# Optimization experiments

Measured on AMD Instinct MI355X. Metric: run time of the kernel, lower is better.

The kernel has to match this reference:

```python
import jax, jax.numpy as jnp
import numpy as np

V, D, F, H, NB, S, B = 16384, 512, 2048, 8, 4, 512, 2
T_STEPS = 3      # config.T: number of PC inference iterations
GAMMA = 0.1      # state-update step size


def _layernorm(x, s, b):
    m = x.mean(-1, keepdims=True)
    v = ((x - m) ** 2).mean(-1, keepdims=True)
    return (x - m) * jax.lax.rsqrt(v + 1e-5) * s + b


def setup_inputs() -> dict:
    key = jax.random.key(0)
    ks = jax.random.split(key, 12)
    r = lambda k, sh: jax.random.normal(k, sh, jnp.float32) * 0.02
    return {
        'word_emb': r(ks[0], (V, D)),
        'pos_emb': r(ks[1], (S, D)),
        'Wq': r(ks[2], (NB, D, D)),
        'Wk': r(ks[3], (NB, D, D)),
        'Wv': r(ks[4], (NB, D, D)),
        'bq': jnp.zeros((NB, D), jnp.float32),
        'bk': jnp.zeros((NB, D), jnp.float32),
        'bv': jnp.zeros((NB, D), jnp.float32),
        'Wo': r(ks[5], (NB, D, D)),
        'bo': jnp.zeros((NB, D), jnp.float32),
        'ln1_s': jnp.ones((NB, D), jnp.float32),
        'ln1_b': jnp.zeros((NB, D), jnp.float32),
        'ln2_s': jnp.ones((NB, D), jnp.float32),
        'ln2_b': jnp.zeros((NB, D), jnp.float32),
        'W1': r(ks[6], (NB, D, F)),
        'b1': jnp.zeros((NB, F), jnp.float32),
        'W2': r(ks[7], (NB, F, D)),
        'b2': jnp.zeros((NB, D), jnp.float32),
        'Wout': r(ks[8], (D, V)),
        'bout': jnp.zeros((V,), jnp.float32),
        'input_ids': jax.random.randint(ks[9], (B, S), 0, V),
        'target_ids': jax.random.randint(ks[10], (B, S), 0, V),
    }


def _forward(word_emb, pos_emb, Wq, Wk, Wv, bq, bk, bv, Wo, bo,
             ln1_s, ln1_b, ln2_s, ln2_b, W1, b1, W2, b2, Wout, bout,
             input_ids, target_ids):
    Bsz, Sl = input_ids.shape
    dh = D // H
    scale = 1.0 / float(np.sqrt(dh))
    ids = jnp.clip(input_ids, 0, V - 1)
    target = jax.nn.one_hot(jnp.clip(target_ids, 0, V - 1), V, dtype=word_emb.dtype)
    # bottom prediction: word + position embeddings
    mu_emb = word_emb[ids] + pos_emb[jnp.arange(Sl)][None]  # (B,S,D)
    causal = jnp.tril(jnp.ones((Sl, Sl), bool))
    neg = jnp.finfo(word_emb.dtype).min

    def attn(x, b):
        h = _layernorm(x, ln1_s[b], ln1_b[b])
        q = (h @ Wq[b] + bq[b]).reshape(Bsz, Sl, H, dh)
        k = (h @ Wk[b] + bk[b]).reshape(Bsz, Sl, H, dh)
        v = (h @ Wv[b] + bv[b]).reshape(Bsz, Sl, H, dh)
        sc = jnp.einsum('bqhd,bkhd->bhqk', q, k) * scale
        sc = jnp.where(causal, sc, neg)
        a = jax.nn.softmax(sc, axis=-1)
        return jnp.einsum('bhqk,bkhd->bqhd', a, v).reshape(Bsz, Sl, D)

    # generative functions g[l]: x_l -> mu_{l+1}; 4 PC layers per block
    # (pc_qkv->attn ctx, pc_output->Wo, pc_layer1->gelu(fc1), pc_layer2->fc2)
    gs = []
    for b in range(NB):
        gs.append(lambda x, b=b: attn(x, b))
        gs.append(lambda x, b=b: x @ Wo[b] + bo[b])
        gs.append(lambda x, b=b: jax.nn.gelu(_layernorm(x, ln2_s[b], ln2_b[b]) @ W1[b] + b1[b]))
        gs.append(lambda x, b=b: x @ W2[b] + b2[b])
    g_top = lambda x: x @ Wout + bout  # output pc layer -> logits mu

    # init_x: forward sweep sets each latent to its prediction
    xs = [mu_emb]
    for g in gs:
        xs.append(g(xs[-1]))
    L = len(gs)

    # T-step iterative PC inference: eps_l = x_l - mu_l, top clamped to target
    # x_l <- x_l + GAMMA * (J_{g_l}(x_l)^T eps_{l+1} - eps_l)
    for _ in range(T_STEPS):
        preds, vjps = [], []
        for l in range(L):
            mu, vj = jax.vjp(gs[l], xs[l])
            preds.append(mu)
            vjps.append(vj)
        logits, vj_top = jax.vjp(g_top, xs[L])
        eps = [xs[0] - mu_emb] + [xs[l + 1] - preds[l] for l in range(L)]
        eps_top = logits - target
        new_xs = []
        for l in range(L + 1):
            td = vjps[l](eps[l + 1])[0] if l < L else vj_top(eps_top)[0]
            new_xs.append(xs[l] + GAMMA * (td - eps[l]))
        xs = new_xs

    return g_top(xs[L])  # get_mu('linear_output')


def reference(word_emb, pos_emb, Wq, Wk, Wv, bq, bk, bv, Wo, bo,
              ln1_s, ln1_b, ln2_s, ln2_b, W1, b1, W2, b2, Wout, bout,
              input_ids, target_ids):
    return _forward(word_emb, pos_emb, Wq, Wk, Wv, bq, bk, bv, Wo, bo,
                    ln1_s, ln1_b, ln2_s, ln2_b, W1, b1, W2, b2, Wout, bout,
                    input_ids, target_ids)
```

## Files before the change

### kernel.cpp

```cpp
#include <hip/hip_runtime.h>
#include <hip/hip_bf16.h>
#include <math.h>

#define D_   512
#define F_   2048
#define V_   16384
#define H_   8
#define DH_  64
#define S_   512
#define B_   2
#define M_   1024
#define MD_  (M_ * D_)
#define MF_  (M_ * F_)
#define GAMMA_ 0.1f

typedef unsigned int u32;
typedef unsigned short u16;
typedef __attribute__((ext_vector_type(4))) float f32x4;
typedef __attribute__((ext_vector_type(8))) short s16x8;
typedef __attribute__((ext_vector_type(4))) u16 u16x4;
typedef __attribute__((ext_vector_type(8))) u16 u16x8;

__device__ __forceinline__ u16 f2b(float f) {
    __hip_bfloat16 h = __float2bfloat16(f);
    return *reinterpret_cast<u16*>(&h);
}
__device__ __forceinline__ float b2f(u16 v) {
    u32 u = ((u32)v) << 16;
    float f; __builtin_memcpy(&f, &u, 4); return f;
}
__device__ __forceinline__ u16x4 pack4(f32x4 v) {
    u16x4 o; o.x = f2b(v[0]); o.y = f2b(v[1]); o.z = f2b(v[2]); o.w = f2b(v[3]);
    return o;
}

__device__ __forceinline__ void gl_lds16(const void* g, void* l) {
    __builtin_amdgcn_global_load_lds((const __attribute__((address_space(1))) u32*)g,
                                     (__attribute__((address_space(3))) u32*)l, 16, 0, 0);
}

__device__ __forceinline__ float gelu_f(float v) {
    float u = 0.7978845608028654f * (v + 0.044715f * v * v * v);
    return 0.5f * v * (1.f + tanhf(u));
}

__device__ __forceinline__ f32x4 xpose4(f32x4 v, int b) {
#pragma unroll
    for (int s = 1; s < 4; s <<= 1) {
        f32x4 nv;
#pragma unroll
        for (int j = 0; j < 4; ++j) {
            float ex = __shfl_xor(v[j ^ s], s, 64);
            nv[j] = ((b ^ j) & s) ? ex : v[j];
        }
        v = nv;
    }
    return v;
}

__device__ __forceinline__ float wave_sum(float v) {
#pragma unroll
    for (int o = 32; o > 0; o >>= 1) v += __shfl_xor(v, o, 64);
    return v;
}

#define E_F32   0
#define E_GELU  1
#define E_TD    2
#define E_EC2   3
#define E_QKV3  4
#define E_OUT   5
#define E_BF16  6

template<int BK>
__device__ __forceinline__ int swz(int c, int row) {
    if constexpr (BK == 32) return c ^ ((row >> 1) & 3);
    else                    return c ^ (row & 7);
}

template<int BM, int BN, int BK, int FM, int FN, int EPI>
__global__ __launch_bounds__(256)
void mfma_gemm(const u16* __restrict__ A, const u16* __restrict__ B,
               float* __restrict__ Cf, u16* __restrict__ Cb,
               u16* __restrict__ Cb2, u16* __restrict__ Cb3,
               const float* __restrict__ bias,
               int K, int lda, int ldb, int ldc,
               long sC, long sKz, float alpha,
               const float* __restrict__ base, const float* __restrict__ subv,
               const float* __restrict__ cvec, const u16* __restrict__ woutTb,
               const int* __restrict__ tcl,
               float* __restrict__ ebF, u16* __restrict__ ebB)
{
    constexpr int WC = BN / (FN * 16);
    static_assert((BM / (FM * 16)) * WC == 4, "4 waves");
    constexpr int LPR = BK / 8;
    constexpr int RPI = 2048 / BK;
    constexpr int NISS = BM / RPI + BN / RPI;
    __shared__ __align__(16) u16 Asl[3][BM * BK];
    __shared__ __align__(16) u16 Bsl[3][BN * BK];
    const int t = threadIdx.x, l = t & 63, wid = t >> 6;
    const int m0 = blockIdx.y * BM, n0 = blockIdx.x * BN;
    const long z = blockIdx.z;
    A += z * sKz;
    B += z * sKz;
    if (Cf) Cf += z * sC;

    f32x4 acc[FM][FN] = {};
    const int rm = (wid / WC) * (FM * 16), cn = (wid % WC) * (FN * 16);
    const int lr = l & 15, hi = l >> 4;
    const int srl = t / LPR, sc = t % LPR;

    auto stage = [&](int k0, int pb) {
#pragma unroll
        for (int i = 0; i < BM / RPI; ++i) {
            int row = i * RPI + srl;
            gl_lds16(A + (size_t)(m0 + row) * lda + k0 + swz<BK>(sc, row) * 8,
                     &Asl[pb][i * 2048 + t * 8]);
        }
#pragma unroll
        for (int i = 0; i < BN / RPI; ++i) {
            int row = i * RPI + srl;
            gl_lds16(B + (size_t)(n0 + row) * ldb + k0 + swz<BK>(sc, row) * 8,
                     &Bsl[pb][i * 2048 + t * 8]);
        }
    };
    auto compute = [&](int pb) {
#pragma unroll
        for (int kk = 0; kk < BK / 32; ++kk) {
            s16x8 av[FM], bv[FN];
#pragma unroll
            for (int fm = 0; fm < FM; ++fm)
                av[fm] = *(const s16x8*)&Asl[pb][(rm + fm * 16 + lr) * BK + swz<BK>(kk * 4 + hi, lr) * 8];
#pragma unroll
            for (int fn = 0; fn < FN; ++fn)
                bv[fn] = *(const s16x8*)&Bsl[pb][(cn + fn * 16 + lr) * BK + swz<BK>(kk * 4 + hi, lr) * 8];
#pragma unroll
            for (int fm = 0; fm < FM; ++fm)
#pragma unroll
                for (int fn = 0; fn < FN; ++fn)
                    acc[fm][fn] = __builtin_amdgcn_mfma_f32_16x16x32_bf16(av[fm], bv[fn], acc[fm][fn], 0, 0, 0);
        }
    };

    const int nst = K / BK;
    stage(0, 0);
    if (nst > 1) stage(BK, 1);
    int rd = 0, wr = 2;
    for (int s = 0; s < nst; ++s) {
        if (s < nst - 1)
            asm volatile("s_waitcnt vmcnt(%0)" :: "i"(NISS) : "memory");
        else
            asm volatile("s_waitcnt vmcnt(0)" ::: "memory");
        __builtin_amdgcn_s_barrier();
        __builtin_amdgcn_sched_barrier(0);
        compute(rd);
        if (s + 2 < nst) stage((s + 2) * BK, wr);
        rd = (rd + 1 == 3) ? 0 : rd + 1;
        wr = (wr + 1 == 3) ? 0 : wr + 1;
    }

    const int qb = lr & 3, qi = lr >> 2;
#pragma unroll
    for (int fm = 0; fm < FM; ++fm)
#pragma unroll
        for (int fn = 0; fn < FN; ++fn) {
            const int gm = m0 + rm + fm * 16 + hi * 4 + qb;
            const int gn0 = n0 + cn + fn * 16 + qi * 4;
            const size_t idx0 = (size_t)gm * ldc + gn0;
            if constexpr (EPI == E_QKV3) {
                const int gnf = n0 + cn + fn * 16;
                const int sel = gnf >> 9;
                if (sel < 2) {
                    f32x4 v = xpose4(acc[fm][fn], qb);
                    f32x4 bv4 = *(const f32x4*)&bias[gn0];
#pragma unroll
                    for (int j = 0; j < 4; ++j) v[j] += bv4[j];
                    int b = gm >> 9, s = gm & (S_ - 1);
                    int d9 = gn0 & 511, h = d9 >> 6, d = d9 & 63;
                    u16* dst = (sel == 0) ? Cb : Cb2;
                    *(u16x4*)&dst[(((size_t)(b * H_ + h) * S_ + s) << 6) + d] = pack4(v);
                } else {
                    const int gnl = gnf + lr;
                    const int gm0 = m0 + rm + fm * 16 + hi * 4;
                    int b = gm0 >> 9, s0 = gm0 & (S_ - 1);
                    int d9 = gnl & 511, h = d9 >> 6, d = d9 & 63;
                    float bb = bias[gnl];
                    f32x4 v = acc[fm][fn];
#pragma unroll
                    for (int j = 0; j < 4; ++j) v[j] += bb;
                    *(u16x4*)&Cb3[((((size_t)(b * H_ + h)) << 6) + d) * S_ + s0] = pack4(v);
                }
            } else {
                f32x4 v = xpose4(acc[fm][fn], qb);
                if constexpr (EPI == E_F32) {
#pragma unroll
                    for (int j = 0; j < 4; ++j) v[j] *= alpha;
                    if (bias) {
                        f32x4 bv4 = *(const f32x4*)&bias[gn0];
#pragma unroll
                        for (int j = 0; j < 4; ++j) v[j] += bv4[j];
                    }
                    *(f32x4*)&Cf[idx0] = v;
                    if (Cb) *(u16x4*)&Cb[idx0] = pack4(v);
                } else if constexpr (EPI == E_OUT) {
                    f32x4 bv4 = *(const f32x4*)&bias[gn0];
#pragma unroll
                    for (int j = 0; j < 4; ++j) v[j] += bv4[j];
                    *(f32x4*)&Cf[idx0] = v;
                } else if constexpr (EPI == E_GELU) {
                    f32x4 bv4 = *(const f32x4*)&bias[gn0];
#pragma unroll
                    for (int j = 0; j < 4; ++j) v[j] = gelu_f(v[j] + bv4[j]);
                    *(u16x4*)&Cb[idx0] = pack4(v);
                } else if constexpr (EPI == E_TD) {
                    const int tc = tcl[gm];
                    f32x4 cv4 = *(const f32x4*)&cvec[gn0];
                    f32x4 ba4 = *(const f32x4*)&base[idx0];
                    u16x4 gv = *(const u16x4*)&woutTb[(size_t)tc * D_ + gn0];
                    f32x4 dlt, o2;
#pragma unroll
                    for (int j = 0; j < 4; ++j)
                        dlt[j] = GAMMA_ * (v[j] + cv4[j] - b2f(gv[j]));
                    if (subv) {
                        f32x4 sv4 = *(const f32x4*)&subv[idx0];
#pragma unroll
                        for (int j = 0; j < 4; ++j) dlt[j] -= GAMMA_ * sv4[j];
                    }
#pragma unroll
                    for (int j = 0; j < 4; ++j) o2[j] = ba4[j] + dlt[j];
                    if (Cf) *(f32x4*)&Cf[idx0] = o2;
                    *(u16x4*)&Cb[idx0] = pack4(o2);
                    if (ebF) *(f32x4*)&ebF[idx0] = dlt;
                    if (ebB) *(u16x4*)&ebB[idx0] = pack4(dlt);
                } else if constexpr (EPI == E_EC2) {
                    f32x4 ba4 = *(const f32x4*)&base[idx0];
                    f32x4 sv4 = *(const f32x4*)&subv[idx0];
#pragma unroll
                    for (int j = 0; j < 4; ++j) v[j] = ba4[j] - sv4[j] - GAMMA_ * v[j];
                    *(f32x4*)&Cf[idx0] = v;
                } else if constexpr (EPI == E_BF16) {
                    *(u16x4*)&Cb[idx0] = pack4(v);
                }
            }
        }
}

__global__ __launch_bounds__(256)
void flash_attn(const u16* __restrict__ q, const u16* __restrict__ k,
                const u16* __restrict__ vT, u16* __restrict__ ctx)
{
    __shared__ __align__(16) u16 Ks[3][64 * 64];
    __shared__ __align__(16) u16 Vs[3][64 * 64];
    __shared__ __align__(16) u16 Ps[4][16 * 64];
    const int t = threadIdx.x, l = t & 63, w = t >> 6;
    const int qt = blockIdx.x, z = blockIdx.y;
    const int bb = z >> 3, hh = z & 7;
    const int lr = l & 15, hi = l >> 4;
    const u16* qp = q + (((size_t)z * S_ + qt * 64 + w * 16) << 6);
    const u16* kp = k + ((size_t)z * S_ << 6);
    const u16* vp = vT + (((size_t)z) << 6) * S_;

    const s16x8 aq0 = *(const s16x8*)&qp[lr * 64 + hi * 8];
    const s16x8 aq1 = *(const s16x8*)&qp[lr * 64 + 32 + hi * 8];

    f32x4 o[4] = {};
    float m[4], ls[4];
#pragma unroll
    for (int r = 0; r < 4; ++r) { m[r] = -3.0e38f; ls[r] = 0.f; }
    const int qrow = qt * 64 + w * 16 + hi * 4;
    const int srow = t >> 3, scl = t & 7;
    const int cg1 = (scl ^ (srow & 7)) * 8;
    const int srow2 = srow + 32;
    const int cg2 = (scl ^ (srow2 & 7)) * 8;
    const int sw7 = (lr & 7);

    auto stage = [&](int j, int pb) {
        gl_lds16(kp + ((size_t)(j * 64 + srow) << 6) + cg1, &Ks[pb][t * 8]);
        gl_lds16(vp + (size_t)srow * S_ + j * 64 + cg1, &Vs[pb][t * 8]);
        gl_lds16(kp + ((size_t)(j * 64 + srow2) << 6) + cg2, &Ks[pb][(t + 256) * 8]);
        gl_lds16(vp + (size_t)srow2 * S_ + j * 64 + cg2, &Vs[pb][(t + 256) * 8]);
    };

    stage(0, 0);
    if (qt > 0) stage(1, 1);
    int rd = 0, wr = 2;
    for (int j = 0; j <= qt; ++j) {
        if (j < qt) asm volatile("s_waitcnt vmcnt(4)" ::: "memory");
        else        asm volatile("s_waitcnt vmcnt(0)" ::: "memory");
        __builtin_amdgcn_s_barrier();
        __builtin_amdgcn_sched_barrier(0);

        float pv[4][4];
#pragma unroll
        for (int fn = 0; fn < 4; ++fn) {
            f32x4 acc = {};
            acc = __builtin_amdgcn_mfma_f32_16x16x32_bf16(aq0,
                    *(const s16x8*)&Ks[rd][((fn * 16 + lr) << 6) + ((hi ^ sw7) * 8)], acc, 0, 0, 0);
            acc = __builtin_amdgcn_mfma_f32_16x16x32_bf16(aq1,
                    *(const s16x8*)&Ks[rd][((fn * 16 + lr) << 6) + (((hi + 4) ^ sw7) * 8)], acc, 0, 0, 0);
#pragma unroll
            for (int r = 0; r < 4; ++r) pv[fn][r] = acc[r] * 0.125f;
        }
        if (j == qt) {
#pragma unroll
            for (int fn = 0; fn < 4; ++fn) {
                int col = j * 64 + fn * 16 + lr;
#pragma unroll
                for (int r = 0; r < 4; ++r)
                    if (col > qrow + r) pv[fn][r] = -3.0e38f;
            }
        }
        float sc[4], rs[4];
#pragma unroll
        for (int r = 0; r < 4; ++r) {
            float x = fmaxf(fmaxf(pv[0][r], pv[1][r]), fmaxf(pv[2][r], pv[3][r]));
#pragma unroll
            for (int off = 1; off < 16; off <<= 1) x = fmaxf(x, __shfl_xor(x, off, 64));
            float nm = fmaxf(m[r], x);
            sc[r] = expf(m[r] - nm);
            m[r] = nm;
            rs[r] = 0.f;
        }
#pragma unroll
        for (int fn = 0; fn < 4; ++fn)
#pragma unroll
            for (int r = 0; r < 4; ++r) {
                float p = expf(pv[fn][r] - m[r]);
                pv[fn][r] = p;
                rs[r] += p;
            }
#pragma unroll
        for (int r = 0; r < 4; ++r) {
#pragma unroll
            for (int off = 1; off < 16; off <<= 1) rs[r] += __shfl_xor(rs[r], off, 64);
            ls[r] = ls[r] * sc[r] + rs[r];
        }
#pragma unroll
        for (int fn = 0; fn < 4; ++fn)
#pragma unroll
            for (int r = 0; r < 4; ++r) o[fn][r] *= sc[r];
#pragma unroll
        for (int fn = 0; fn < 4; ++fn)
#pragma unroll
            for (int r = 0; r < 4; ++r) {
                int qr = hi * 4 + r;
                int ci = (2 * fn + (lr >> 3)) ^ (qr & 7);
                Ps[w][qr * 64 + ci * 8 + (lr & 7)] = f2b(pv[fn][r]);
            }
#pragma unroll
        for (int ks = 0; ks < 2; ++ks) {
            const s16x8 pa = *(const s16x8*)&Ps[w][lr * 64 + (((4 * ks + hi) ^ sw7) * 8)];
#pragma unroll
            for (int fn = 0; fn < 4; ++fn)
                o[fn] = __builtin_amdgcn_mfma_f32_16x16x32_bf16(pa,
                        *(const s16x8*)&Vs[rd][((fn * 16 + lr) << 6) + (((hi + 4 * ks) ^ sw7) * 8)], o[fn], 0, 0, 0);
        }
        if (j + 2 <= qt) stage(j + 2, wr);
        rd = (rd + 1 == 3) ? 0 : rd + 1;
        wr = (wr + 1 == 3) ? 0 : wr + 1;
    }
    float inv[4];
#pragma unroll
    for (int r = 0; r < 4; ++r) inv[r] = 1.f / ls[r];
    u16* cp = ctx + ((size_t)(bb * S_ + qt * 64 + w * 16) * D_) + hh * 64;
    const int qb = lr & 3, qi = lr >> 2;
#pragma unroll
    for (int fn = 0; fn < 4; ++fn) {
        f32x4 v = o[fn];
#pragma unroll
        for (int r = 0; r < 4; ++r) v[r] *= inv[r];
        v = xpose4(v, qb);
        *(u16x4*)&cp[(size_t)(hi * 4 + qb) * D_ + fn * 16 + qi * 4] = pack4(v);
    }
}

__global__ __launch_bounds__(256)
void prep0(const float* __restrict__ bq, const float* __restrict__ bk,
           const float* __restrict__ bv, const int* __restrict__ target_ids,
           float* __restrict__ qkvb, int* __restrict__ tcl, float* __restrict__ cvec)
{
    int i = blockIdx.x * 256 + threadIdx.x;
    if (i < 512) cvec[i] = 0.f;
    else if (i < 1536) {
        int mm = i - 512;
        int v = target_ids[mm];
        tcl[mm] = v < 0 ? 0 : (v > V_ - 1 ? V_ - 1 : v);
    } else if (i < 1536 + 6144) {
        int j = i - 1536;
        int b = j / 1536, r = j - b * 1536;
        qkvb[j] = (r < 512) ? bq[b * 512 + r]
                : (r < 1024) ? bk[b * 512 + r - 512] : bv[b * 512 + r - 1024];
    }
}

__global__ __launch_bounds__(256)
void mega_prep(const float* __restrict__ Wq, const float* __restrict__ Wk,
               const float* __restrict__ Wv, const float* __restrict__ Wo,
               const float* __restrict__ W1, const float* __restrict__ W2,
               const float* __restrict__ Wout, const float* __restrict__ bout,
               u16* __restrict__ wqkvT, u16* __restrict__ woT, u16* __restrict__ w1T,
               u16* __restrict__ w2T, u16* __restrict__ woutT,
               u16* __restrict__ woutD, float* __restrict__ cvec)
{
    __shared__ float tile[64][65];
    const int g = blockIdx.x, t = threadIdx.x;

    const float* in = nullptr;
    u16 *outT = nullptr, *outC = nullptr;
    int R = 512, C = 512, tx = 0, ty = 0;
    bool doCvec = false;

    if (g < 768) {
        int sel = g / 256, rem = g % 256, zz = rem >> 6, tl = rem & 63;
        in = (sel == 0 ? Wq : sel == 1 ? Wk : Wv) + (size_t)zz * 262144;
        outT = wqkvT + (size_t)zz * 786432 + sel * 262144;
        tx = tl & 7; ty = tl >> 3;
    } else if (g < 1024) {
        int rem = g - 768, zz = rem >> 6, tl = rem & 63;
        in = Wo + (size_t)zz * 262144; outT = woT + (size_t)zz * 262144;
        tx = tl & 7; ty = tl >> 3;
    } else if (g < 2048) {
        int rem = g - 1024, zz = rem >> 8, tl = rem & 255;
        in = W1 + (size_t)zz * 1048576; outT = w1T + (size_t)zz * 1048576;
        C = 2048; tx = tl & 31; ty = tl >> 5;
    } else if (g < 3072) {
        int rem = g - 2048, zz = rem >> 8, tl = rem & 255;
        in = W2 + (size_t)zz * 1048576; outT = w2T + (size_t)zz * 1048576;
        R = 2048; tx = tl & 7; ty = tl >> 3;
    } else {
        int tl = g - 3072;
        in = Wout; outT = woutT; outC = woutD; doCvec = true;
        C = 16384; tx = tl & 255; ty = tl >> 8;
    }

    const int r0 = ty * 64, c0 = tx * 64;
#pragma unroll
    for (int p = 0; p < 4; ++p) {
        int row = p * 16 + (t >> 4), col = (t & 15) * 4;
        float4 v = *(const float4*)&in[(size_t)(r0 + row) * C + c0 + col];
        tile[row][col] = v.x; tile[row][col + 1] = v.y;
        tile[row][col + 2] = v.z; tile[row][col + 3] = v.w;
        if (outC) {
            f32x4 fv; fv[0] = v.x; fv[1] = v.y; fv[2] = v.z; fv[3] = v.w;
            *(u16x4*)&outC[(size_t)(r0 + row) * C + c0 + col] = pack4(fv);
        }
    }
    __syncthreads();
#pragma unroll
    for (int p = 0; p < 2; ++p) {
        int orow = p * 32 + (t >> 3), oc = (t & 7) * 8;
        u16x8 o;
#pragma unroll
        for (int j = 0; j < 8; ++j) o[j] = f2b(tile[oc + j][orow]);
        *(u16x8*)&outT[(size_t)(c0 + orow) * R + r0 + oc] = o;
    }
    if (doCvec) {
        int r = t >> 2, qq = t & 3;
        float s = 0.f;
#pragma unroll
        for (int i = 0; i < 16; ++i)
            s += tile[r][qq * 16 + i] * bout[c0 + qq * 16 + i];
        s += __shfl_xor(s, 1, 64);
        s += __shfl_xor(s, 2, 64);
        if (qq == 0) atomicAdd(&cvec[r0 + r], s);
    }
}

__global__ void gred_kernel(const float* __restrict__ P, u16* __restrict__ G)
{
    int i = blockIdx.x * blockDim.x + threadIdx.x;
    if (i < D_ * D_) {
        float s = 0.f;
#pragma unroll
        for (int zz = 0; zz < 16; ++zz) s += P[(size_t)zz * D_ * D_ + i];
        G[i] = f2b(s);
    }
}

__global__ void embed_kernel(const float4* __restrict__ we, const float4* __restrict__ pe,
                             const int* __restrict__ ids, float4* __restrict__ o)
{
    int t = blockIdx.x * blockDim.x + threadIdx.x;
    int d4 = t & 127, row = t >> 7;
    int ss = row & (S_ - 1);
    int id = ids[row];
    id = id < 0 ? 0 : (id > V_ - 1 ? V_ - 1 : id);
    float4 a = we[(size_t)id * 128 + d4];
    float4 b = pe[(size_t)ss * 128 + d4];
    o[(size_t)row * 128 + d4] = make_float4(a.x + b.x, a.y + b.y, a.z + b.z, a.w + b.w);
}

__global__ __launch_bounds__(256)
void ln_fwd_kernel(const float* __restrict__ x, const float* __restrict__ s,
                   const float* __restrict__ bb, u16* __restrict__ h)
{
    const int l = threadIdx.x & 63, w = threadIdx.x >> 6;
    const int row = blockIdx.x * 4 + w;
    const float* xr = x + (size_t)row * D_;
    const int c0 = l * 8;
    float4 a = *(const float4*)&xr[c0];
    float4 b = *(const float4*)&xr[c0 + 4];
    float sum = a.x + a.y + a.z + a.w + b.x + b.y + b.z + b.w;
    float mu = wave_sum(sum) * (1.f / D_);
    float d0 = a.x - mu, d1 = a.y - mu, d2 = a.z - mu, d3 = a.w - mu;
    float d4 = b.x - mu, d5 = b.y - mu, d6 = b.z - mu, d7 = b.w - mu;
    float vs = d0*d0 + d1*d1 + d2*d2 + d3*d3 + d4*d4 + d5*d5 + d6*d6 + d7*d7;
    float var = wave_sum(vs) * (1.f / D_);
    float r = rsqrtf(var + 1e-5f);
    float4 s0 = *(const float4*)&s[c0], s1 = *(const float4*)&s[c0 + 4];
    float4 b0 = *(const float4*)&bb[c0], b1 = *(const float4*)&bb[c0 + 4];
    u16* hr = h + (size_t)row * D_;
    f32x4 o0, o1;
    o0[0] = d0 * r * s0.x + b0.x; o0[1] = d1 * r * s0.y + b0.y;
    o0[2] = d2 * r * s0.z + b0.z; o0[3] = d3 * r * s0.w + b0.w;
    o1[0] = d4 * r * s1.x + b1.x; o1[1] = d5 * r * s1.y + b1.y;
    o1[2] = d6 * r * s1.z + b1.z; o1[3] = d7 * r * s1.w + b1.w;
    *(u16x4*)&hr[c0] = pack4(o0);
    *(u16x4*)&hr[c0 + 4] = pack4(o1);
}

extern "C" void kernel_launch(void* const* d_in, const int* in_sizes, int n_in,
                              void* d_out, int out_size, void* d_ws, size_t ws_size,
                              hipStream_t stream)
{
    (void)in_sizes; (void)n_in; (void)out_size;
    const float* Wq  = (const float*)d_in[2];
    const float* Wk  = (const float*)d_in[3];
    const float* Wv  = (const float*)d_in[4];
    const float* bq  = (const float*)d_in[5];
    const float* bk  = (const float*)d_in[6];
    const float* bv  = (const float*)d_in[7];
    const float* Wo  = (const float*)d_in[8];
    const float* bo  = (const float*)d_in[9];
    const float* ln1_s = (const float*)d_in[10];
    const float* ln1_b = (const float*)d_in[11];
    const float* ln2_s = (const float*)d_in[12];
    const float* ln2_b = (const float*)d_in[13];
    const float* W1  = (const float*)d_in[14];
    const float* b1  = (const float*)d_in[15];
    const float* W2  = (const float*)d_in[16];
    const float* b2  = (const float*)d_in[17];
    const float* Wout = (const float*)d_in[18];
    const float* bout = (const float*)d_in[19];
    const int* input_ids  = (const int*)d_in[20];
    const int* target_ids = (const int*)d_in[21];
    float* out = (float*)d_out;

    char* wsb = (char*)d_ws;
    size_t off = 0;
    auto alloc = [&](size_t bytes) -> void* {
        off = (off + 255) & ~(size_t)255;
        void* p = wsb + off; off += bytes; return p;
    };
    u16* wqkvT = (u16*)alloc((size_t)4 * 1536 * D_ * 2);
    u16* woT   = (u16*)alloc((size_t)4 * D_ * D_ * 2);
    u16* w1T   = (u16*)alloc((size_t)4 * D_ * F_ * 2);
    u16* w2T   = (u16*)alloc((size_t)4 * D_ * F_ * 2);
    u16* woutT = (u16*)alloc((size_t)V_ * D_ * 2);
    u16* G_b   = (u16*)alloc((size_t)D_ * D_ * 2);
    u16* H2_b  = (u16*)alloc((size_t)D_ * D_ * 2);
    float* qkvb = (float*)alloc((size_t)4 * 1536 * 4);
    float* bufB = (float*)alloc((size_t)MD_ * 4);
    u16* h_b    = (u16*)alloc((size_t)MD_ * 2);
    u16* gelu_b = (u16*)alloc((size_t)MF_ * 2);
    u16* x16_b  = (u16*)alloc((size_t)MD_ * 2);
    float* cvec = (float*)alloc(D_ * 4);
    int* tcl    = (int*)alloc(M_ * 4);
    size_t uStart = (off + 255) & ~(size_t)255;
    off = uStart;
    u16* woutD   = (u16*)alloc((size_t)V_ * D_ * 2);
    float* Gpart = (float*)alloc((size_t)16 * D_ * D_ * 4);
    size_t endG = off;
    off = uStart;
    u16* q_b   = (u16*)alloc((size_t)MD_ * 2);
    u16* k_b   = (u16*)alloc((size_t)MD_ * 2);
    u16* v_b   = (u16*)alloc((size_t)MD_ * 2);
    u16* ctx_b = (u16*)alloc((size_t)MD_ * 2);
    size_t endA = off;
    off = uStart;
    float* xA  = (float*)alloc((size_t)MD_ * 4);
    float* xB  = (float*)alloc((size_t)MD_ * 4);
    float* eb  = (float*)alloc((size_t)MD_ * 4);
    float* ec  = (float*)alloc((size_t)MD_ * 4);
    u16* xA_b  = (u16*)alloc((size_t)MD_ * 2);
    u16* xB_b  = (u16*)alloc((size_t)MD_ * 2);
    u16* xC_b  = (u16*)alloc((size_t)MD_ * 2);
    u16* eb_b  = (u16*)alloc((size_t)MD_ * 2);
    size_t endT = off;
    size_t need = endG > endA ? endG : endA;
    if (endT > need) need = endT;
    if (need > ws_size) return;

    dim3 blk(256);
    const long NL = 0;
    #define GZ nullptr, nullptr, nullptr, nullptr, nullptr, nullptr, nullptr

    prep0<<<dim3(32), blk, 0, stream>>>(bq, bk, bv, target_ids, qkvb, tcl, cvec);
    mega_prep<<<dim3(5120), blk, 0, stream>>>(Wq, Wk, Wv, Wo, W1, W2, Wout, bout,
        wqkvT, woT, w1T, w2T, woutT, woutD, cvec);
    mfma_gemm<128, 128, 64, 4, 4, E_F32><<<dim3(4, 4, 16), blk, 0, stream>>>(
        woutD, woutD, Gpart, nullptr, nullptr, nullptr, nullptr, 1024, V_, V_, D_,
        (long)D_ * D_, 1024, 1.f, GZ);
    gred_kernel<<<dim3(1024), blk, 0, stream>>>(Gpart, G_b);
    mfma_gemm<64, 64, 64, 2, 2, E_BF16><<<dim3(8, 8, 1), blk, 0, stream>>>(
        w2T + (size_t)3 * D_ * F_, w2T + (size_t)3 * D_ * F_, nullptr, H2_b,
        nullptr, nullptr, nullptr, F_, F_, F_, D_, NL, NL, 1.f, GZ);

    embed_kernel<<<dim3(512), blk, 0, stream>>>((const float4*)d_in[0], (const float4*)d_in[1],
                                                input_ids, (float4*)bufB);
    for (int b = 0; b < 4; ++b) {
        const size_t wDD = (size_t)b * D_ * D_, wDF = (size_t)b * D_ * F_;
        ln_fwd_kernel<<<dim3(M_ / 4), blk, 0, stream>>>(bufB, ln1_s + b * D_, ln1_b + b * D_, h_b);
        mfma_gemm<128, 64, 64, 4, 2, E_QKV3><<<dim3(24, 8, 1), blk, 0, stream>>>(
            h_b, wqkvT + (size_t)b * 1536 * 512, nullptr, q_b, k_b, v_b,
            qkvb + b * 1536, D_, D_, D_, 0, NL, NL, 1.f, GZ);
        flash_attn<<<dim3(8, 16), blk, 0, stream>>>(q_b, k_b, v_b, ctx_b);
        mfma_gemm<64, 64, 64, 2, 2, E_F32><<<dim3(8, 16, 1), blk, 0, stream>>>(
            ctx_b, woT + wDD, bufB, nullptr, nullptr, nullptr, bo + b * D_,
            D_, D_, D_, D_, NL, NL, 1.f, GZ);
        ln_fwd_kernel<<<dim3(M_ / 4), blk, 0, stream>>>(bufB, ln2_s + b * D_, ln2_b + b * D_, h_b);
        mfma_gemm<64, 64, 64, 2, 2, E_GELU><<<dim3(32, 16, 1), blk, 0, stream>>>(
            h_b, w1T + wDF, nullptr, gelu_b, nullptr, nullptr, b1 + b * F_,
            D_, D_, D_, F_, NL, NL, 1.f, GZ);
        mfma_gemm<64, 64, 64, 2, 2, E_F32><<<dim3(8, 16, 1), blk, 0, stream>>>(
            gelu_b, w2T + wDF, bufB, (b == 3) ? x16_b : nullptr, nullptr, nullptr, b2 + b * D_,
            F_, F_, F_, D_, NL, NL, 1.f, GZ);
    }

    mfma_gemm<64, 64, 64, 2, 2, E_TD><<<dim3(8, 16, 1), blk, 0, stream>>>(
        x16_b, G_b, xA, xA_b, nullptr, nullptr, nullptr, D_, D_, D_, D_, NL, NL, 1.f,
        bufB, nullptr, cvec, woutT, tcl, eb, eb_b);
    mfma_gemm<64, 64, 64, 2, 2, E_TD><<<dim3(8, 16, 1), blk, 0, stream>>>(
        xA_b, G_b, xB, xB_b, nullptr, nullptr, nullptr, D_, D_, D_, D_, NL, NL, 1.f,
        xA, eb, cvec, woutT, tcl, nullptr, nullptr);
    mfma_gemm<64, 64, 64, 2, 2, E_EC2><<<dim3(8, 16, 1), blk, 0, stream>>>(
        eb_b, H2_b, ec, nullptr, nullptr, nullptr, nullptr, D_, D_, D_, D_, NL, NL, 1.f,
        xB, bufB, nullptr, nullptr, nullptr, nullptr, nullptr);
    mfma_gemm<64, 64, 64, 2, 2, E_TD><<<dim3(8, 16, 1), blk, 0, stream>>>(
        xB_b, G_b, nullptr, xC_b, nullptr, nullptr, nullptr, D_, D_, D_, D_, NL, NL, 1.f,
        xB, ec, cvec, woutT, tcl, nullptr, nullptr);
    mfma_gemm<128, 256, 32, 4, 8, E_OUT><<<dim3(64, 8, 1), blk, 0, stream>>>(
        xC_b, woutT, out, nullptr, nullptr, nullptr, bout, D_, D_, D_, V_, NL, NL, 1.f, GZ);
    #undef GZ
}
```

Before: 423.8 us.

## Shrink tiles for more blocks, halve flash-attn block, fold prep kernels

Flash attention now runs 128-thread blocks, each covering 32 query rows instead of 64, which doubles the grid from 128 to 256 blocks. Several small D×D GEMMs move to 32×64 tiles and the output GEMM moves to 128×128 tiles, again to launch more blocks and fill the CUs. The prep0 kernel is folded into mega_prep as one extra block. The cvec bias contraction moves out of the atomics in mega_prep into the G-reduction kernel as a wave-level dot product. This trades per-block data reuse for higher occupancy and fewer launches. In flash attention, blocks that share a 64-key tile now load it redundantly.

```diff
diff --git a/kernel.cpp b/kernel.cpp
--- a/kernel.cpp
+++ b/kernel.cpp
@@ -245,18 +245,18 @@
         }
 }
 
-__global__ __launch_bounds__(256)
+__global__ __launch_bounds__(128)
 void flash_attn(const u16* __restrict__ q, const u16* __restrict__ k,
                 const u16* __restrict__ vT, u16* __restrict__ ctx)
 {
     __shared__ __align__(16) u16 Ks[3][64 * 64];
     __shared__ __align__(16) u16 Vs[3][64 * 64];
-    __shared__ __align__(16) u16 Ps[4][16 * 64];
+    __shared__ __align__(16) u16 Ps[2][16 * 64];
     const int t = threadIdx.x, l = t & 63, w = t >> 6;
     const int qt = blockIdx.x, z = blockIdx.y;
     const int bb = z >> 3, hh = z & 7;
     const int lr = l & 15, hi = l >> 4;
-    const u16* qp = q + (((size_t)z * S_ + qt * 64 + w * 16) << 6);
+    const u16* qp = q + (((size_t)z * S_ + qt * 32 + w * 16) << 6);
     const u16* kp = k + ((size_t)z * S_ << 6);
     const u16* vp = vT + (((size_t)z) << 6) * S_;
 
@@ -267,26 +267,29 @@
     float m[4], ls[4];
 #pragma unroll
     for (int r = 0; r < 4; ++r) { m[r] = -3.0e38f; ls[r] = 0.f; }
-    const int qrow = qt * 64 + w * 16 + hi * 4;
+    const int qrow = qt * 32 + w * 16 + hi * 4;
     const int srow = t >> 3, scl = t & 7;
-    const int cg1 = (scl ^ (srow & 7)) * 8;
-    const int srow2 = srow + 32;
-    const int cg2 = (scl ^ (srow2 & 7)) * 8;
+    const int cg = (scl ^ (srow & 7)) * 8;
     const int sw7 = (lr & 7);
+    const int jmax = qt >> 1;
 
     auto stage = [&](int j, int pb) {
-        gl_lds16(kp + ((size_t)(j * 64 + srow) << 6) + cg1, &Ks[pb][t * 8]);
-        gl_lds16(vp + (size_t)srow * S_ + j * 64 + cg1, &Vs[pb][t * 8]);
-        gl_lds16(kp + ((size_t)(j * 64 + srow2) << 6) + cg2, &Ks[pb][(t + 256) * 8]);
-        gl_lds16(vp + (size_t)srow2 * S_ + j * 64 + cg2, &Vs[pb][(t + 256) * 8]);
+#pragma unroll
+        for (int i = 0; i < 4; ++i)
+            gl_lds16(kp + ((size_t)(j * 64 + i * 16 + srow) << 6) + cg,
+                     &Ks[pb][i * 1024 + t * 8]);
+#pragma unroll
+        for (int i = 0; i < 4; ++i)
+            gl_lds16(vp + (size_t)(i * 16 + srow) * S_ + j * 64 + cg,
+                     &Vs[pb][i * 1024 + t * 8]);
     };
 
     stage(0, 0);
-    if (qt > 0) stage(1, 1);
+    if (jmax > 0) stage(1, 1);
     int rd = 0, wr = 2;
-    for (int j = 0; j <= qt; ++j) {
-        if (j < qt) asm volatile("s_waitcnt vmcnt(4)" ::: "memory");
-        else        asm volatile("s_waitcnt vmcnt(0)" ::: "memory");
+    for (int j = 0; j <= jmax; ++j) {
+        if (j < jmax) asm volatile("s_waitcnt vmcnt(8)" ::: "memory");
+        else          asm volatile("s_waitcnt vmcnt(0)" ::: "memory");
         __builtin_amdgcn_s_barrier();
         __builtin_amdgcn_sched_barrier(0);
 
@@ -301,7 +304,7 @@
 #pragma unroll
             for (int r = 0; r < 4; ++r) pv[fn][r] = acc[r] * 0.125f;
         }
-        if (j == qt) {
+        if (j == jmax) {
 #pragma unroll
             for (int fn = 0; fn < 4; ++fn) {
                 int col = j * 64 + fn * 16 + lr;
@@ -355,14 +358,14 @@
                 o[fn] = __builtin_amdgcn_mfma_f32_16x16x32_bf16(pa,
                         *(const s16x8*)&Vs[rd][((fn * 16 + lr) << 6) + (((hi + 4 * ks) ^ sw7) * 8)], o[fn], 0, 0, 0);
         }
-        if (j + 2 <= qt) stage(j + 2, wr);
+        if (j + 2 <= jmax) stage(j + 2, wr);
         rd = (rd + 1 == 3) ? 0 : rd + 1;
         wr = (wr + 1 == 3) ? 0 : wr + 1;
     }
     float inv[4];
 #pragma unroll
     for (int r = 0; r < 4; ++r) inv[r] = 1.f / ls[r];
-    u16* cp = ctx + ((size_t)(bb * S_ + qt * 64 + w * 16) * D_) + hh * 64;
+    u16* cp = ctx + ((size_t)(bb * S_ + qt * 32 + w * 16) * D_) + hh * 64;
     const int qb = lr & 3, qi = lr >> 2;
 #pragma unroll
     for (int fn = 0; fn < 4; ++fn) {
@@ -371,25 +374,6 @@
         for (int r = 0; r < 4; ++r) v[r] *= inv[r];
         v = xpose4(v, qb);
         *(u16x4*)&cp[(size_t)(hi * 4 + qb) * D_ + fn * 16 + qi * 4] = pack4(v);
-    }
-}
-
-__global__ __launch_bounds__(256)
-void prep0(const float* __restrict__ bq, const float* __restrict__ bk,
-           const float* __restrict__ bv, const int* __restrict__ target_ids,
-           float* __restrict__ qkvb, int* __restrict__ tcl, float* __restrict__ cvec)
-{
-    int i = blockIdx.x * 256 + threadIdx.x;
-    if (i < 512) cvec[i] = 0.f;
-    else if (i < 1536) {
-        int mm = i - 512;
-        int v = target_ids[mm];
-        tcl[mm] = v < 0 ? 0 : (v > V_ - 1 ? V_ - 1 : v);
-    } else if (i < 1536 + 6144) {
-        int j = i - 1536;
-        int b = j / 1536, r = j - b * 1536;
-        qkvb[j] = (r < 512) ? bq[b * 512 + r]
-                : (r < 1024) ? bk[b * 512 + r - 512] : bv[b * 512 + r - 1024];
     }
 }
 
@@ -397,10 +381,12 @@
 void mega_prep(const float* __restrict__ Wq, const float* __restrict__ Wk,
                const float* __restrict__ Wv, const float* __restrict__ Wo,
                const float* __restrict__ W1, const float* __restrict__ W2,
-               const float* __restrict__ Wout, const float* __restrict__ bout,
+               const float* __restrict__ Wout,
+               const float* __restrict__ bq, const float* __restrict__ bk,
+               const float* __restrict__ bv, const int* __restrict__ target_ids,
                u16* __restrict__ wqkvT, u16* __restrict__ woT, u16* __restrict__ w1T,
                u16* __restrict__ w2T, u16* __restrict__ woutT,
-               u16* __restrict__ woutD, float* __restrict__ cvec)
+               u16* __restrict__ woutD, float* __restrict__ qkvb, int* __restrict__ tcl)
 {
     __shared__ float tile[64][65];
     const int g = blockIdx.x, t = threadIdx.x;
@@ -408,7 +394,6 @@
     const float* in = nullptr;
     u16 *outT = nullptr, *outC = nullptr;
     int R = 512, C = 512, tx = 0, ty = 0;
-    bool doCvec = false;
 
     if (g < 768) {
         int sel = g / 256, rem = g % 256, zz = rem >> 6, tl = rem & 63;
@@ -427,10 +412,21 @@
         int rem = g - 2048, zz = rem >> 8, tl = rem & 255;
         in = W2 + (size_t)zz * 1048576; outT = w2T + (size_t)zz * 1048576;
         R = 2048; tx = tl & 7; ty = tl >> 3;
+    } else if (g < 5120) {
+        int tl = g - 3072;
+        in = Wout; outT = woutT; outC = woutD;
+        C = 16384; tx = tl & 255; ty = tl >> 8;
     } else {
-        int tl = g - 3072;
-        in = Wout; outT = woutT; outC = woutD; doCvec = true;
-        C = 16384; tx = tl & 255; ty = tl >> 8;
+        for (int i = t; i < M_; i += 256) {
+            int v = target_ids[i];
+            tcl[i] = v < 0 ? 0 : (v > V_ - 1 ? V_ - 1 : v);
+        }
+        for (int i = t; i < 4 * 1536; i += 256) {
+            int b = i / 1536, j = i - b * 1536;
+            qkvb[i] = (j < 512) ? bq[b * 512 + j]
+                    : (j < 1024) ? bk[b * 512 + j - 512] : bv[b * 512 + j - 1024];
+        }
+        return;
     }
 
     const int r0 = ty * 64, c0 = tx * 64;
@@ -454,26 +450,34 @@
         for (int j = 0; j < 8; ++j) o[j] = f2b(tile[oc + j][orow]);
         *(u16x8*)&outT[(size_t)(c0 + orow) * R + r0 + oc] = o;
     }
-    if (doCvec) {
-        int r = t >> 2, qq = t & 3;
-        float s = 0.f;
-#pragma unroll
-        for (int i = 0; i < 16; ++i)
-            s += tile[r][qq * 16 + i] * bout[c0 + qq * 16 + i];
-        s += __shfl_xor(s, 1, 64);
-        s += __shfl_xor(s, 2, 64);
-        if (qq == 0) atomicAdd(&cvec[r0 + r], s);
-    }
-}
-
-__global__ void gred_kernel(const float* __restrict__ P, u16* __restrict__ G)
+}
+
+__global__ __launch_bounds__(256)
+void gredcvec(const float* __restrict__ P, u16* __restrict__ G,
+              const u16* __restrict__ woutD, const float* __restrict__ bout,
+              float* __restrict__ cvec)
 {
-    int i = blockIdx.x * blockDim.x + threadIdx.x;
-    if (i < D_ * D_) {
+    const int blk = blockIdx.x;
+    if (blk < 1024) {
+        int i = blk * 256 + threadIdx.x;
         float s = 0.f;
 #pragma unroll
         for (int zz = 0; zz < 16; ++zz) s += P[(size_t)zz * D_ * D_ + i];
         G[i] = f2b(s);
+    } else {
+        const int w = threadIdx.x >> 6, l = threadIdx.x & 63;
+        const int d = (blk - 1024) * 4 + w;
+        float s = 0.f;
+        for (int it = 0; it < 32; ++it) {
+            int base = it * 512 + l * 8;
+            u16x8 wv = *(const u16x8*)&woutD[(size_t)d * V_ + base];
+            float4 b0 = *(const float4*)&bout[base];
+            float4 b1 = *(const float4*)&bout[base + 4];
+            s += b2f(wv[0]) * b0.x + b2f(wv[1]) * b0.y + b2f(wv[2]) * b0.z + b2f(wv[3]) * b0.w
+               + b2f(wv[4]) * b1.x + b2f(wv[5]) * b1.y + b2f(wv[6]) * b1.z + b2f(wv[7]) * b1.w;
+        }
+        s = wave_sum(s);
+        if (l == 0) cvec[d] = s;
     }
 }
 
@@ -595,14 +599,13 @@
     const long NL = 0;
     #define GZ nullptr, nullptr, nullptr, nullptr, nullptr, nullptr, nullptr
 
-    prep0<<<dim3(32), blk, 0, stream>>>(bq, bk, bv, target_ids, qkvb, tcl, cvec);
-    mega_prep<<<dim3(5120), blk, 0, stream>>>(Wq, Wk, Wv, Wo, W1, W2, Wout, bout,
-        wqkvT, woT, w1T, w2T, woutT, woutD, cvec);
+    mega_prep<<<dim3(5121), blk, 0, stream>>>(Wq, Wk, Wv, Wo, W1, W2, Wout,
+        bq, bk, bv, target_ids, wqkvT, woT, w1T, w2T, woutT, woutD, qkvb, tcl);
     mfma_gemm<128, 128, 64, 4, 4, E_F32><<<dim3(4, 4, 16), blk, 0, stream>>>(
         woutD, woutD, Gpart, nullptr, nullptr, nullptr, nullptr, 1024, V_, V_, D_,
         (long)D_ * D_, 1024, 1.f, GZ);
-    gred_kernel<<<dim3(1024), blk, 0, stream>>>(Gpart, G_b);
-    mfma_gemm<64, 64, 64, 2, 2, E_BF16><<<dim3(8, 8, 1), blk, 0, stream>>>(
+    gredcvec<<<dim3(1152), blk, 0, stream>>>(Gpart, G_b, woutD, bout, cvec);
+    mfma_gemm<32, 64, 64, 1, 2, E_BF16><<<dim3(8, 16, 1), blk, 0, stream>>>(
         w2T + (size_t)3 * D_ * F_, w2T + (size_t)3 * D_ * F_, nullptr, H2_b,
         nullptr, nullptr, nullptr, F_, F_, F_, D_, NL, NL, 1.f, GZ);
 
@@ -611,35 +614,35 @@
     for (int b = 0; b < 4; ++b) {
         const size_t wDD = (size_t)b * D_ * D_, wDF = (size_t)b * D_ * F_;
         ln_fwd_kernel<<<dim3(M_ / 4), blk, 0, stream>>>(bufB, ln1_s + b * D_, ln1_b + b * D_, h_b);
-        mfma_gemm<128, 64, 64, 4, 2, E_QKV3><<<dim3(24, 8, 1), blk, 0, stream>>>(
+        mfma_gemm<64, 64, 64, 2, 2, E_QKV3><<<dim3(24, 16, 1), blk, 0, stream>>>(
             h_b, wqkvT + (size_t)b * 1536 * 512, nullptr, q_b, k_b, v_b,
             qkvb + b * 1536, D_, D_, D_, 0, NL, NL, 1.f, GZ);
-        flash_attn<<<dim3(8, 16), blk, 0, stream>>>(q_b, k_b, v_b, ctx_b);
-        mfma_gemm<64, 64, 64, 2, 2, E_F32><<<dim3(8, 16, 1), blk, 0, stream>>>(
+        flash_attn<<<dim3(16, 16), dim3(128), 0, stream>>>(q_b, k_b, v_b, ctx_b);
+        mfma_gemm<32, 64, 64, 1, 2, E_F32><<<dim3(8, 32, 1), blk, 0, stream>>>(
             ctx_b, woT + wDD, bufB, nullptr, nullptr, nullptr, bo + b * D_,
             D_, D_, D_, D_, NL, NL, 1.f, GZ);
         ln_fwd_kernel<<<dim3(M_ / 4), blk, 0, stream>>>(bufB, ln2_s + b * D_, ln2_b + b * D_, h_b);
         mfma_gemm<64, 64, 64, 2, 2, E_GELU><<<dim3(32, 16, 1), blk, 0, stream>>>(
             h_b, w1T + wDF, nullptr, gelu_b, nullptr, nullptr, b1 + b * F_,
             D_, D_, D_, F_, NL, NL, 1.f, GZ);
-        mfma_gemm<64, 64, 64, 2, 2, E_F32><<<dim3(8, 16, 1), blk, 0, stream>>>(
+        mfma_gemm<32, 64, 64, 1, 2, E_F32><<<dim3(8, 32, 1), blk, 0, stream>>>(
             gelu_b, w2T + wDF, bufB, (b == 3) ? x16_b : nullptr, nullptr, nullptr, b2 + b * D_,
             F_, F_, F_, D_, NL, NL, 1.f, GZ);
     }
 
-    mfma_gemm<64, 64, 64, 2, 2, E_TD><<<dim3(8, 16, 1), blk, 0, stream>>>(
+    mfma_gemm<32, 64, 64, 1, 2, E_TD><<<dim3(8, 32, 1), blk, 0, stream>>>(
         x16_b, G_b, xA, xA_b, nullptr, nullptr, nullptr, D_, D_, D_, D_, NL, NL, 1.f,
         bufB, nullptr, cvec, woutT, tcl, eb, eb_b);
-    mfma_gemm<64, 64, 64, 2, 2, E_TD><<<dim3(8, 16, 1), blk, 0, stream>>>(
+    mfma_gemm<32, 64, 64, 1, 2, E_TD><<<dim3(8, 32, 1), blk, 0, stream>>>(
         xA_b, G_b, xB, xB_b, nullptr, nullptr, nullptr, D_, D_, D_, D_, NL, NL, 1.f,
         xA, eb, cvec, woutT, tcl, nullptr, nullptr);
-    mfma_gemm<64, 64, 64, 2, 2, E_EC2><<<dim3(8, 16, 1), blk, 0, stream>>>(
+    mfma_gemm<32, 64, 64, 1, 2, E_EC2><<<dim3(8, 32, 1), blk, 0, stream>>>(
         eb_b, H2_b, ec, nullptr, nullptr, nullptr, nullptr, D_, D_, D_, D_, NL, NL, 1.f,
         xB, bufB, nullptr, nullptr, nullptr, nullptr, nullptr);
-    mfma_gemm<64, 64, 64, 2, 2, E_TD><<<dim3(8, 16, 1), blk, 0, stream>>>(
+    mfma_gemm<32, 64, 64, 1, 2, E_TD><<<dim3(8, 32, 1), blk, 0, stream>>>(
         xB_b, G_b, nullptr, xC_b, nullptr, nullptr, nullptr, D_, D_, D_, D_, NL, NL, 1.f,
         xB, ec, cvec, woutT, tcl, nullptr, nullptr);
-    mfma_gemm<128, 256, 32, 4, 8, E_OUT><<<dim3(64, 8, 1), blk, 0, stream>>>(
+    mfma_gemm<128, 128, 32, 4, 4, E_OUT><<<dim3(128, 8, 1), blk, 0, stream>>>(
         xC_b, woutT, out, nullptr, nullptr, nullptr, bout, D_, D_, D_, V_, NL, NL, 1.f, GZ);
     #undef GZ
 }
```

After: 386.9 us. 1.1x faster.
